# Kernel tuning notes

Hardware: AMD Instinct MI355X
Metric: run time of the kernel (lower is better)

Reference implementation:

```python
import jax, jax.numpy as jnp
import numpy as np

N, F, C, H, D = 32768, 128, 4, 8, 32
DM = H * D  # 256, d_model
E, B = 65536, 8192


def _pe():
    # sinusoidal positional encoding over the chain dimension, shape [C, DM]
    pos = jnp.arange(C, dtype=jnp.float32)[:, None]
    di = jnp.arange(0, DM, 2, dtype=jnp.float32)[None, :]
    div = 10000.0 ** (di / DM)
    pe = jnp.zeros((C, DM), jnp.float32)
    pe = pe.at[:, 0::2].set(jnp.sin(pos / div))
    pe = pe.at[:, 1::2].set(jnp.cos(pos / div))
    return pe


def _leaky(v):
    return jnp.where(v >= 0, v, 0.2 * v)


def setup_inputs() -> dict:
    key = jax.random.key(0)
    ks = jax.random.split(key, 6)
    x = jax.random.normal(ks[0], (N, F), jnp.float32)
    edge_index = jax.random.randint(ks[1], (2, E), 0, N)
    bridge_index = jax.random.randint(ks[2], (2, B), 0, N)
    W_in = jax.random.normal(ks[3], (DM, F), jnp.float32) * 0.05       # linear_input.weight
    double_attn = jax.random.normal(ks[4], (1, C * H, D), jnp.float32) * 0.1
    W_res = jax.random.normal(ks[5], (C * DM, F), jnp.float32) * 0.05  # residual_linear.weight
    bias = jnp.zeros((C * DM,), jnp.float32)
    prelu_w = jnp.float32(0.25)  # nn.PReLU default
    return {"x": x, "edge_index": edge_index, "bridge_index": bridge_index,
            "W_in": W_in, "double_attn": double_attn, "W_res": W_res,
            "bias": bias, "prelu_w": prelu_w}


def reference(x, edge_index, bridge_index, W_in, double_attn, W_res, bias, prelu_w):
    n = x.shape[0]
    # project + chain positional encoding -> [n, C, H, D]
    xl = x @ W_in.T                                   # [n, DM]
    xr = (xl[:, None, :] + _pe()[None]).reshape(n, C, H, D)

    src_bond, dst_bond = edge_index[0], edge_index[1]
    bond_attn = _leaky(xr[src_bond] + xr[dst_bond])   # [E, C, H, D]

    src_bridge, dst_bridge = bridge_index[0], bridge_index[1]
    ch = jnp.arange(C)
    prev_ch = jnp.clip(ch - 1, 0, None)
    next_ch = jnp.clip(ch + 1, None, C - 1)
    src2dst = _leaky(xr[dst_bridge] + xr[src_bridge][:, next_ch]).at[:, -1].set(0.0)
    dst2src = _leaky(xr[src_bridge] + xr[dst_bridge][:, prev_ch]).at[:, 0].set(0.0)

    full_src = jnp.concatenate([src_bond, src_bridge, dst_bridge])   # [Et]
    full_dst = jnp.concatenate([dst_bond, dst_bridge, src_bridge])   # [Et]
    x_src = jnp.concatenate([xr[src_bond], xr[src_bridge], xr[dst_bridge]], axis=0).reshape(-1, C * H, D)
    edge_attn = jnp.concatenate([bond_attn, src2dst, dst2src], axis=0).reshape(-1, C * H, D)

    scores = (double_attn * edge_attn).sum(-1)        # [Et, C*H]
    exp_s = jnp.exp(scores - scores.max())            # global-max stabilized, as in original
    denom = jax.ops.segment_sum(exp_s, full_dst, num_segments=n)     # [n, C*H]
    alpha = exp_s / (denom[full_dst] + 1e-16)

    # NOTE: faithful to original bug - x_src (per-edge, len Et) indexed by NODE ids
    proj = x_src[full_src] * alpha[..., None]         # [Et, C*H, D]
    out = jax.ops.segment_sum(proj, full_dst, num_segments=n)        # [n, C*H, D]

    out = out + (x @ W_res.T).reshape(n, C * H, D)    # residual
    out = out.reshape(n, C * H * D) + bias            # concat + bias
    out = jnp.where(out >= 0, out, prelu_w * out)     # PReLU
    return out
```

## Files before the change

### kernel.cpp

```cpp
#include <hip/hip_runtime.h>
#include <math.h>

#define N_NODES 32768
#define F_IN    128
#define C_CH    4
#define H_HEADS 8
#define D_DIM   32
#define DM      256
#define E_BOND  65536
#define B_BRIDGE 8192
#define ET      (E_BOND + 2*B_BRIDGE)
#define OUTC    1024
#define CAP     24
#define NCOLS   1280

#define WS_XL      0u
#define WS_XLB     33554432u
#define WS_PE      50331648u
#define WS_SCORES  50335744u
#define WS_BUCKET2 60821504u
#define WS_CNT     67112960u
#define WS_GMAX    67244032u
#define WS_RESID   67248128u
#define WS_XB      134356992u
#define WS_WC      142745600u

typedef __attribute__((ext_vector_type(8))) short bf16x8;
typedef __attribute__((ext_vector_type(4))) float f32x4;
typedef __attribute__((ext_vector_type(4))) _Float16 f16x4;

__device__ __forceinline__ unsigned enc_f32(float f) {
    unsigned u = __float_as_uint(f);
    return (u & 0x80000000u) ? ~u : (u | 0x80000000u);
}
__device__ __forceinline__ float dec_f32(unsigned u) {
    return (u & 0x80000000u) ? __uint_as_float(u & 0x7fffffffu) : __uint_as_float(~u);
}
__device__ __forceinline__ float leaky(float v) { return v >= 0.f ? v : 0.2f*v; }
__device__ __forceinline__ ushort f2bf(float f) {
    unsigned u = __float_as_uint(f);
    unsigned r = (u + 0x7fffu + ((u >> 16) & 1u)) >> 16;
    return (ushort)r;
}
__device__ __forceinline__ float bf2f(ushort u) {
    return __uint_as_float((unsigned)u << 16);
}

__device__ __forceinline__ void edge_decode(int e, const int* __restrict__ ei,
                                            const int* __restrict__ bi,
                                            int& nA, int& nB, int& tp) {
    if (e < E_BOND)               { nA = ei[e]; nB = ei[E_BOND + e]; tp = 0; }
    else if (e < E_BOND+B_BRIDGE) { int i = e - E_BOND;
                                    nA = bi[B_BRIDGE + i]; nB = bi[i]; tp = 1; }
    else                          { int i = e - E_BOND - B_BRIDGE;
                                    nA = bi[i]; nB = bi[B_BRIDGE + i]; tp = 2; }
}

__global__ void pe_init_kernel(float* __restrict__ pe, unsigned* __restrict__ gmax) {
    int tid = threadIdx.x;
    int c = tid >> 8, p = tid & 255;
    float expo = (float)(p & ~1) * (1.0f/256.0f);
    float div  = powf(10000.0f, expo);
    float arg  = (float)c / div;
    pe[tid] = (p & 1) ? cosf(arg) : sinf(arg);
    if (tid == 0) *gmax = 0u;
}

__global__ __launch_bounds__(256) void cvt_x_kernel(const float* __restrict__ x,
                                                    ushort* __restrict__ xb) {
    const long i = (long)blockIdx.x*256 + threadIdx.x;
    float4 v = ((const float4*)x)[i];
    ushort4 o; o.x = f2bf(v.x); o.y = f2bf(v.y); o.z = f2bf(v.z); o.w = f2bf(v.w);
    ((ushort4*)xb)[i] = o;
}
__global__ __launch_bounds__(256) void cvt_w_kernel(const float* __restrict__ W_in,
                                                    const float* __restrict__ W_res,
                                                    ushort* __restrict__ wc) {
    const int i = blockIdx.x*256 + threadIdx.x;
    float4 v = (i < 8192) ? ((const float4*)W_in)[i] : ((const float4*)W_res)[i - 8192];
    ushort4 o; o.x = f2bf(v.x); o.y = f2bf(v.y); o.z = f2bf(v.z); o.w = f2bf(v.w);
    ((ushort4*)wc)[i] = o;
}

#define LDSK 72
__global__ __launch_bounds__(256) void mfma_gemm(
        const ushort* __restrict__ xb, const ushort* __restrict__ wc,
        float* __restrict__ xl, ushort* __restrict__ xlb,
        _Float16* __restrict__ resid) {
    __shared__ ushort As[128*LDSK];
    __shared__ ushort Bs[128*LDSK];
    const int tid = threadIdx.x;
    const int m0 = blockIdx.x * 128;
    const int n0 = blockIdx.y * 128;
    const int lane = tid & 63, wv = tid >> 6;
    const int wm = wv & 1, wn = wv >> 1;
    const int quad = lane >> 4, l15 = lane & 15;
    const int mbase = wm*64, nbase = wn*64;
    f32x4 acc[4][4] = {};

    for (int kt = 0; kt < 2; ++kt) {
        if (kt) __syncthreads();
#pragma unroll
        for (int i = 0; i < 4; ++i) {
            int c = tid + i*256;
            int row = c >> 3, seg = c & 7;
            *(uint4*)&As[row*LDSK + seg*8] =
                *(const uint4*)(xb + (long)(m0 + row)*F_IN + kt*64 + seg*8);
        }
#pragma unroll
        for (int i = 0; i < 4; ++i) {
            int c = tid + i*256;
            int row = c >> 3, seg = c & 7;
            *(uint4*)&Bs[row*LDSK + seg*8] =
                *(const uint4*)(wc + (long)(n0 + row)*F_IN + kt*64 + seg*8);
        }
        __syncthreads();
#pragma unroll
        for (int ks = 0; ks < 2; ++ks) {
            const int ko = ks*32 + quad*8;
            bf16x8 af[4], bfr[4];
#pragma unroll
            for (int mi = 0; mi < 4; ++mi)
                af[mi] = *(const bf16x8*)&As[(mbase + mi*16 + l15)*LDSK + ko];
#pragma unroll
            for (int ni = 0; ni < 4; ++ni)
                bfr[ni] = *(const bf16x8*)&Bs[(nbase + ni*16 + l15)*LDSK + ko];
#pragma unroll
            for (int mi = 0; mi < 4; ++mi)
#pragma unroll
                for (int ni = 0; ni < 4; ++ni)
                    acc[mi][ni] = __builtin_amdgcn_mfma_f32_16x16x32_bf16(
                        af[mi], bfr[ni], acc[mi][ni], 0, 0, 0);
        }
    }

    if (n0 < DM) {
#pragma unroll
        for (int mi = 0; mi < 4; ++mi) {
            const int mrow = m0 + mbase + mi*16 + quad*4;
#pragma unroll
            for (int ni = 0; ni < 4; ++ni) {
                const int col = n0 + nbase + ni*16 + l15;
#pragma unroll
                for (int r = 0; r < 4; ++r) {
                    float v = acc[mi][ni][r];
                    xl [(long)(mrow + r)*DM + col] = v;
                    xlb[(long)(mrow + r)*DM + col] = f2bf(v);
                }
            }
        }
    } else {
        const int coloff = n0 - DM;
#pragma unroll
        for (int mi = 0; mi < 4; ++mi) {
            const int mrow = m0 + mbase + mi*16 + quad*4;
#pragma unroll
            for (int ni = 0; ni < 4; ++ni) {
                const int col = coloff + nbase + ni*16 + l15;
#pragma unroll
                for (int r = 0; r < 4; ++r)
                    resid[(long)(mrow + r)*OUTC + col] = (_Float16)acc[mi][ni][r];
            }
        }
    }
}

__global__ __launch_bounds__(256) void build_kernel(
        const int* __restrict__ ei, const int* __restrict__ bi,
        int* __restrict__ counts, int2* __restrict__ bucket2) {
    const int e = blockIdx.x*256 + threadIdx.x;
    if (e >= ET) return;
    int nA, nB, tp;
    edge_decode(e, ei, bi, nA, nB, tp);
    const int dst = (tp == 0) ? nB : nA;
    const int fs  = (tp == 0) ? nA : nB;
    const int g   = ei[fs];
    int slot = atomicAdd(&counts[dst], 1);
    if (slot < CAP) bucket2[dst*CAP + slot] = make_int2(e, g);
}

__global__ __launch_bounds__(256) void scores_kernel(
        const ushort* __restrict__ xlb, const float* __restrict__ pe,
        const int* __restrict__ ei, const int* __restrict__ bi,
        const float* __restrict__ datt, float* __restrict__ scores,
        unsigned* __restrict__ gmax) {
    const int tid = threadIdx.x;
    const int l = tid & 63, wv = tid >> 6;
    const int pos = l * 4;
    const int h = l >> 3, dq = l & 7;

    float4 pe4[4], w4[4];
#pragma unroll
    for (int c = 0; c < 4; ++c) {
        pe4[c] = *(const float4*)(pe + c*DM + pos);
        w4[c]  = *(const float4*)(datt + (c*H_HEADS + h)*D_DIM + dq*4);
    }

    float wmax = -1e30f;
    const int wavebase = (blockIdx.x*4 + wv) * 8;
#pragma unroll
    for (int gdx = 0; gdx < 2; ++gdx) {
        const int e0 = wavebase + gdx*4;
        int nA[4], nB[4], tp[4];
#pragma unroll
        for (int j = 0; j < 4; ++j)
            edge_decode(e0 + j, ei, bi, nA[j], nB[j], tp[j]);
        ushort4 ua[4], ub[4];
#pragma unroll
        for (int j = 0; j < 4; ++j) {
            ua[j] = *(const ushort4*)(xlb + (long)nA[j]*DM + pos);
            ub[j] = *(const ushort4*)(xlb + (long)nB[j]*DM + pos);
        }
#pragma unroll
        for (int j = 0; j < 4; ++j) {
            const int e = e0 + j, t = tp[j];
            float sx = bf2f(ua[j].x) + bf2f(ub[j].x);
            float sy = bf2f(ua[j].y) + bf2f(ub[j].y);
            float sz = bf2f(ua[j].z) + bf2f(ub[j].z);
            float sw = bf2f(ua[j].w) + bf2f(ub[j].w);

            float p[4];
#pragma unroll
            for (int c = 0; c < 4; ++c) {
                int cB = (t == 0) ? c : (t == 1 ? (c+1 < 3 ? c+1 : 3)
                                               : (c-1 > 0 ? c-1 : 0));
                bool z = (t == 1 && c == 3) || (t == 2 && c == 0);
                float4 pa = pe4[c];
                float4 pb = (cB == 0) ? pe4[0] : (cB == 1) ? pe4[1]
                           : (cB == 2) ? pe4[2] : pe4[3];
                float v0 = leaky(sx + pa.x + pb.x);
                float v1 = leaky(sy + pa.y + pb.y);
                float v2 = leaky(sz + pa.z + pb.z);
                float v3 = leaky(sw + pa.w + pb.w);
                float d = w4[c].x*v0 + w4[c].y*v1 + w4[c].z*v2 + w4[c].w*v3;
                p[c] = z ? 0.f : d;
                p[c] += __shfl_xor(p[c], 1);
                p[c] += __shfl_xor(p[c], 2);
                p[c] += __shfl_xor(p[c], 4);
            }
            float val = (dq == 0) ? p[0] : (dq == 1) ? p[1] : (dq == 2) ? p[2] : p[3];
            if (dq < 4) scores[(long)e*32 + dq*8 + h] = val;
            wmax = fmaxf(wmax, fmaxf(fmaxf(p[0], p[1]), fmaxf(p[2], p[3])));
        }
    }

    wmax = fmaxf(wmax, __shfl_xor(wmax, 8));
    wmax = fmaxf(wmax, __shfl_xor(wmax, 16));
    wmax = fmaxf(wmax, __shfl_xor(wmax, 32));
    __shared__ float sm[4];
    if (l == 0) sm[wv] = wmax;
    __syncthreads();
    if (tid == 0) {
        float mm = fmaxf(fmaxf(sm[0], sm[1]), fmaxf(sm[2], sm[3]));
        atomicMax(gmax, enc_f32(mm));
    }
}

__global__ __launch_bounds__(256) void alpha_kernel(
        const int* __restrict__ counts, const int2* __restrict__ bucket2,
        const unsigned* __restrict__ gmax, float* __restrict__ scores) {
    const int t = threadIdx.x;
    const int n = blockIdx.x*8 + (t >> 5);
    const int ch = t & 31;
    const float m = dec_f32(*gmax);
    const int cnt = min(counts[n], CAP);

    float ex[CAP];
    float den = 0.f;
#pragma unroll
    for (int i = 0; i < CAP; ++i) {
        if (i < cnt) {
            int e = bucket2[n*CAP + i].x;
            float v = __expf(scores[(long)e*32 + ch] - m);
            ex[i] = v; den += v;
        }
    }
    const float inv = 1.f / (den + 1e-16f);
#pragma unroll
    for (int i = 0; i < CAP; ++i) {
        if (i < cnt) {
            int e = bucket2[n*CAP + i].x;
            scores[(long)e*32 + ch] = ex[i] * inv;
        }
    }
}

__global__ __launch_bounds__(256) void gather_kernel(
        const float* __restrict__ xl, const float* __restrict__ pe,
        const float* __restrict__ alpha, const int* __restrict__ counts,
        const int2* __restrict__ bucket2, const _Float16* __restrict__ resid,
        const float* __restrict__ bias, const float* __restrict__ pw,
        float* __restrict__ out) {
    const int n = blockIdx.x;
    const int t = threadIdx.x;
    const int ch = t >> 3;
    const int d0 = (t & 7) * 4;
    const int h = ch & 7, c = ch >> 3;
    const int cnt = min(counts[n], CAP);
    const int col = ch*D_DIM + d0;
    const int nb = n*CAP;

    const f16x4 hv = *(const f16x4*)(resid + (long)n*OUTC + col);
    const float4 b = *(const float4*)(bias + col);
    const float w = *pw;
    const float4 pv = *(const float4*)(pe + c*DM + h*D_DIM + d0);

    float4 acc = make_float4(0.f, 0.f, 0.f, 0.f);
    float asum = 0.f;

    for (int i0 = 0; i0 < cnt; i0 += 4) {
#pragma unroll
        for (int j = 0; j < 4; ++j) {
            const int idx = i0 + j;
            const int safe = idx < cnt ? idx : i0;
            int2 eg = bucket2[nb + safe];
            float a = (idx < cnt) ? alpha[(long)eg.x*32 + ch] : 0.f;
            float4 xv = *(const float4*)(xl + (long)eg.y*DM + h*D_DIM + d0);
            acc.x += a*xv.x; acc.y += a*xv.y; acc.z += a*xv.z; acc.w += a*xv.w;
            asum += a;
        }
    }
    acc.x += asum*pv.x; acc.y += asum*pv.y; acc.z += asum*pv.z; acc.w += asum*pv.w;

    float r0 = acc.x + (float)hv.x + b.x;
    float r1 = acc.y + (float)hv.y + b.y;
    float r2 = acc.z + (float)hv.z + b.z;
    float r3 = acc.w + (float)hv.w + b.w;
    r0 = r0 >= 0.f ? r0 : w*r0;
    r1 = r1 >= 0.f ? r1 : w*r1;
    r2 = r2 >= 0.f ? r2 : w*r2;
    r3 = r3 >= 0.f ? r3 : w*r3;
    *(float4*)(out + (long)n*OUTC + col) = make_float4(r0, r1, r2, r3);
}

extern "C" void kernel_launch(void* const* d_in, const int* in_sizes, int n_in,
                              void* d_out, int out_size, void* d_ws, size_t ws_size,
                              hipStream_t stream) {
    const float* x     = (const float*)d_in[0];
    const int*   ei    = (const int*)d_in[1];
    const int*   bi    = (const int*)d_in[2];
    const float* W_in  = (const float*)d_in[3];
    const float* datt  = (const float*)d_in[4];
    const float* W_res = (const float*)d_in[5];
    const float* bias  = (const float*)d_in[6];
    const float* pw    = (const float*)d_in[7];
    float* out = (float*)d_out;
    char*  ws  = (char*)d_ws;

    float*     xl      = (float*)(ws + WS_XL);
    ushort*    xlb     = (ushort*)(ws + WS_XLB);
    float*     pe      = (float*)(ws + WS_PE);
    float*     scores  = (float*)(ws + WS_SCORES);
    int2*      bucket2 = (int2*)(ws + WS_BUCKET2);
    int*       counts  = (int*)(ws + WS_CNT);
    unsigned*  gmax    = (unsigned*)(ws + WS_GMAX);
    _Float16*  resid   = (_Float16*)(ws + WS_RESID);
    ushort*    xb      = (ushort*)(ws + WS_XB);
    ushort*    wc      = (ushort*)(ws + WS_WC);

    hipMemsetAsync(counts, 0, (size_t)N_NODES*4, stream);
    pe_init_kernel<<<1, 1024, 0, stream>>>(pe, gmax);
    cvt_x_kernel<<<(N_NODES*F_IN/4)/256, 256, 0, stream>>>(x, xb);
    cvt_w_kernel<<<(NCOLS*F_IN/4 + 255)/256, 256, 0, stream>>>(W_in, W_res, wc);
    build_kernel<<<(ET+255)/256, 256, 0, stream>>>(ei, bi, counts, bucket2);
    {
        dim3 grid(N_NODES/128, NCOLS/128);
        mfma_gemm<<<grid, 256, 0, stream>>>(xb, wc, xl, xlb, resid);
    }
    scores_kernel<<<2560, 256, 0, stream>>>(xlb, pe, ei, bi, datt, scores, gmax);
    alpha_kernel<<<N_NODES/8, 256, 0, stream>>>(counts, bucket2, gmax, scores);
    gather_kernel<<<N_NODES, 256, 0, stream>>>(xl, pe, scores, counts, bucket2,
                                               resid, bias, pw, out);
}
```

Measured before the change: 345.6 us.

## Fuse score, softmax and gather into one per-node kernel with local max

Replaces the separate scores, alpha and gather kernels with a single node-centric kernel that computes edge scores for each destination's bucket, does the softmax in shared memory, and aggregates. The bucket now stores source/dest node ids and edge type, so the global per-edge scores buffer and the global atomic max are removed. Softmax stabilization uses a per-node max instead of the global max, which is mathematically equivalent. Normalization is applied once after accumulation. In exchange, the score phase per block has low parallelism for small degrees.

```diff
diff --git a/kernel.cpp b/kernel.cpp
--- a/kernel.cpp
+++ b/kernel.cpp
@@ -17,25 +17,16 @@
 #define WS_XL      0u
 #define WS_XLB     33554432u
 #define WS_PE      50331648u
-#define WS_SCORES  50335744u
-#define WS_BUCKET2 60821504u
-#define WS_CNT     67112960u
-#define WS_GMAX    67244032u
-#define WS_RESID   67248128u
-#define WS_XB      134356992u
-#define WS_WC      142745600u
+#define WS_BUCKET  50335744u
+#define WS_CNT     62918656u
+#define WS_RESID   63049728u
+#define WS_XB      130158592u
+#define WS_WC      138547200u
 
 typedef __attribute__((ext_vector_type(8))) short bf16x8;
 typedef __attribute__((ext_vector_type(4))) float f32x4;
 typedef __attribute__((ext_vector_type(4))) _Float16 f16x4;
 
-__device__ __forceinline__ unsigned enc_f32(float f) {
-    unsigned u = __float_as_uint(f);
-    return (u & 0x80000000u) ? ~u : (u | 0x80000000u);
-}
-__device__ __forceinline__ float dec_f32(unsigned u) {
-    return (u & 0x80000000u) ? __uint_as_float(u & 0x7fffffffu) : __uint_as_float(~u);
-}
 __device__ __forceinline__ float leaky(float v) { return v >= 0.f ? v : 0.2f*v; }
 __device__ __forceinline__ ushort f2bf(float f) {
     unsigned u = __float_as_uint(f);
@@ -56,14 +47,13 @@
                                     nA = bi[i]; nB = bi[B_BRIDGE + i]; tp = 2; }
 }
 
-__global__ void pe_init_kernel(float* __restrict__ pe, unsigned* __restrict__ gmax) {
+__global__ void pe_init_kernel(float* __restrict__ pe) {
     int tid = threadIdx.x;
     int c = tid >> 8, p = tid & 255;
     float expo = (float)(p & ~1) * (1.0f/256.0f);
     float div  = powf(10000.0f, expo);
     float arg  = (float)c / div;
     pe[tid] = (p & 1) ? cosf(arg) : sinf(arg);
-    if (tid == 0) *gmax = 0u;
 }
 
 __global__ __launch_bounds__(256) void cvt_x_kernel(const float* __restrict__ x,
@@ -167,7 +157,7 @@
 
 __global__ __launch_bounds__(256) void build_kernel(
         const int* __restrict__ ei, const int* __restrict__ bi,
-        int* __restrict__ counts, int2* __restrict__ bucket2) {
+        int* __restrict__ counts, int4* __restrict__ bucket4) {
     const int e = blockIdx.x*256 + threadIdx.x;
     if (e >= ET) return;
     int nA, nB, tp;
@@ -176,55 +166,50 @@
     const int fs  = (tp == 0) ? nA : nB;
     const int g   = ei[fs];
     int slot = atomicAdd(&counts[dst], 1);
-    if (slot < CAP) bucket2[dst*CAP + slot] = make_int2(e, g);
-}
-
-__global__ __launch_bounds__(256) void scores_kernel(
-        const ushort* __restrict__ xlb, const float* __restrict__ pe,
-        const int* __restrict__ ei, const int* __restrict__ bi,
-        const float* __restrict__ datt, float* __restrict__ scores,
-        unsigned* __restrict__ gmax) {
-    const int tid = threadIdx.x;
-    const int l = tid & 63, wv = tid >> 6;
-    const int pos = l * 4;
-    const int h = l >> 3, dq = l & 7;
-
-    float4 pe4[4], w4[4];
-#pragma unroll
-    for (int c = 0; c < 4; ++c) {
-        pe4[c] = *(const float4*)(pe + c*DM + pos);
-        w4[c]  = *(const float4*)(datt + (c*H_HEADS + h)*D_DIM + dq*4);
-    }
-
-    float wmax = -1e30f;
-    const int wavebase = (blockIdx.x*4 + wv) * 8;
-#pragma unroll
-    for (int gdx = 0; gdx < 2; ++gdx) {
-        const int e0 = wavebase + gdx*4;
-        int nA[4], nB[4], tp[4];
-#pragma unroll
-        for (int j = 0; j < 4; ++j)
-            edge_decode(e0 + j, ei, bi, nA[j], nB[j], tp[j]);
-        ushort4 ua[4], ub[4];
-#pragma unroll
-        for (int j = 0; j < 4; ++j) {
-            ua[j] = *(const ushort4*)(xlb + (long)nA[j]*DM + pos);
-            ub[j] = *(const ushort4*)(xlb + (long)nB[j]*DM + pos);
-        }
-#pragma unroll
-        for (int j = 0; j < 4; ++j) {
-            const int e = e0 + j, t = tp[j];
-            float sx = bf2f(ua[j].x) + bf2f(ub[j].x);
-            float sy = bf2f(ua[j].y) + bf2f(ub[j].y);
-            float sz = bf2f(ua[j].z) + bf2f(ub[j].z);
-            float sw = bf2f(ua[j].w) + bf2f(ub[j].w);
+    if (slot < CAP) bucket4[(long)dst*CAP + slot] = make_int4(nA, nB, g, tp);
+}
+
+__global__ __launch_bounds__(256) void node_kernel(
+        const float* __restrict__ xl, const ushort* __restrict__ xlb,
+        const float* __restrict__ pe, const float* __restrict__ datt,
+        const int* __restrict__ counts, const int4* __restrict__ bucket4,
+        const _Float16* __restrict__ resid, const float* __restrict__ bias,
+        const float* __restrict__ pw, float* __restrict__ out) {
+    __shared__ float s_sc[CAP][32];
+    __shared__ int   s_g[CAP];
+    __shared__ float s_inv[32];
+
+    const int n = blockIdx.x;
+    const int t = threadIdx.x;
+    const int l = t & 63, wv = t >> 6;
+    const int cnt = min(counts[n], CAP);
+
+    {
+        const int pos = l * 4;
+        const int h8 = l >> 3, dq = l & 7;
+        float4 pe4[4], w4[4];
+#pragma unroll
+        for (int c = 0; c < 4; ++c) {
+            pe4[c] = *(const float4*)(pe + c*DM + pos);
+            w4[c]  = *(const float4*)(datt + (c*H_HEADS + h8)*D_DIM + dq*4);
+        }
+        for (int i = wv; i < cnt; i += 4) {
+            const int4 ed = bucket4[(long)n*CAP + i];
+            if (l == 0) s_g[i] = ed.z;
+            const int tp = ed.w;
+            ushort4 ua = *(const ushort4*)(xlb + (long)ed.x*DM + pos);
+            ushort4 ub = *(const ushort4*)(xlb + (long)ed.y*DM + pos);
+            float sx = bf2f(ua.x) + bf2f(ub.x);
+            float sy = bf2f(ua.y) + bf2f(ub.y);
+            float sz = bf2f(ua.z) + bf2f(ub.z);
+            float sw = bf2f(ua.w) + bf2f(ub.w);
 
             float p[4];
 #pragma unroll
             for (int c = 0; c < 4; ++c) {
-                int cB = (t == 0) ? c : (t == 1 ? (c+1 < 3 ? c+1 : 3)
-                                               : (c-1 > 0 ? c-1 : 0));
-                bool z = (t == 1 && c == 3) || (t == 2 && c == 0);
+                int cB = (tp == 0) ? c : (tp == 1 ? (c+1 < 3 ? c+1 : 3)
+                                                  : (c-1 > 0 ? c-1 : 0));
+                bool z = (tp == 1 && c == 3) || (tp == 2 && c == 0);
                 float4 pa = pe4[c];
                 float4 pb = (cB == 0) ? pe4[0] : (cB == 1) ? pe4[1]
                            : (cB == 2) ? pe4[2] : pe4[3];
@@ -238,94 +223,53 @@
                 p[c] += __shfl_xor(p[c], 2);
                 p[c] += __shfl_xor(p[c], 4);
             }
-            float val = (dq == 0) ? p[0] : (dq == 1) ? p[1] : (dq == 2) ? p[2] : p[3];
-            if (dq < 4) scores[(long)e*32 + dq*8 + h] = val;
-            wmax = fmaxf(wmax, fmaxf(fmaxf(p[0], p[1]), fmaxf(p[2], p[3])));
-        }
-    }
-
-    wmax = fmaxf(wmax, __shfl_xor(wmax, 8));
-    wmax = fmaxf(wmax, __shfl_xor(wmax, 16));
-    wmax = fmaxf(wmax, __shfl_xor(wmax, 32));
-    __shared__ float sm[4];
-    if (l == 0) sm[wv] = wmax;
+            if (dq < 4) {
+                float val = (dq == 0) ? p[0] : (dq == 1) ? p[1]
+                           : (dq == 2) ? p[2] : p[3];
+                s_sc[i][dq*8 + h8] = val;
+            }
+        }
+    }
     __syncthreads();
-    if (tid == 0) {
-        float mm = fmaxf(fmaxf(sm[0], sm[1]), fmaxf(sm[2], sm[3]));
-        atomicMax(gmax, enc_f32(mm));
-    }
-}
-
-__global__ __launch_bounds__(256) void alpha_kernel(
-        const int* __restrict__ counts, const int2* __restrict__ bucket2,
-        const unsigned* __restrict__ gmax, float* __restrict__ scores) {
-    const int t = threadIdx.x;
-    const int n = blockIdx.x*8 + (t >> 5);
-    const int ch = t & 31;
-    const float m = dec_f32(*gmax);
-    const int cnt = min(counts[n], CAP);
-
-    float ex[CAP];
-    float den = 0.f;
-#pragma unroll
-    for (int i = 0; i < CAP; ++i) {
-        if (i < cnt) {
-            int e = bucket2[n*CAP + i].x;
-            float v = __expf(scores[(long)e*32 + ch] - m);
-            ex[i] = v; den += v;
-        }
-    }
-    const float inv = 1.f / (den + 1e-16f);
-#pragma unroll
-    for (int i = 0; i < CAP; ++i) {
-        if (i < cnt) {
-            int e = bucket2[n*CAP + i].x;
-            scores[(long)e*32 + ch] = ex[i] * inv;
-        }
-    }
-}
-
-__global__ __launch_bounds__(256) void gather_kernel(
-        const float* __restrict__ xl, const float* __restrict__ pe,
-        const float* __restrict__ alpha, const int* __restrict__ counts,
-        const int2* __restrict__ bucket2, const _Float16* __restrict__ resid,
-        const float* __restrict__ bias, const float* __restrict__ pw,
-        float* __restrict__ out) {
-    const int n = blockIdx.x;
-    const int t = threadIdx.x;
+
+    if (t < 32) {
+        float m = -1e30f;
+        for (int i = 0; i < cnt; ++i) m = fmaxf(m, s_sc[i][t]);
+        float den = 0.f;
+        for (int i = 0; i < cnt; ++i) {
+            float v = __expf(s_sc[i][t] - m);
+            s_sc[i][t] = v;
+            den += v;
+        }
+        s_inv[t] = 1.f / (den + 1e-16f);
+    }
+    __syncthreads();
+
     const int ch = t >> 3;
     const int d0 = (t & 7) * 4;
-    const int h = ch & 7, c = ch >> 3;
-    const int cnt = min(counts[n], CAP);
+    const int hh = ch & 7, cc = ch >> 3;
+    const int dmoff = hh*D_DIM + d0;
     const int col = ch*D_DIM + d0;
-    const int nb = n*CAP;
 
     const f16x4 hv = *(const f16x4*)(resid + (long)n*OUTC + col);
     const float4 b = *(const float4*)(bias + col);
     const float w = *pw;
-    const float4 pv = *(const float4*)(pe + c*DM + h*D_DIM + d0);
+    const float4 pv = *(const float4*)(pe + cc*DM + dmoff);
 
     float4 acc = make_float4(0.f, 0.f, 0.f, 0.f);
     float asum = 0.f;
-
-    for (int i0 = 0; i0 < cnt; i0 += 4) {
-#pragma unroll
-        for (int j = 0; j < 4; ++j) {
-            const int idx = i0 + j;
-            const int safe = idx < cnt ? idx : i0;
-            int2 eg = bucket2[nb + safe];
-            float a = (idx < cnt) ? alpha[(long)eg.x*32 + ch] : 0.f;
-            float4 xv = *(const float4*)(xl + (long)eg.y*DM + h*D_DIM + d0);
-            acc.x += a*xv.x; acc.y += a*xv.y; acc.z += a*xv.z; acc.w += a*xv.w;
-            asum += a;
-        }
-    }
-    acc.x += asum*pv.x; acc.y += asum*pv.y; acc.z += asum*pv.z; acc.w += asum*pv.w;
-
-    float r0 = acc.x + (float)hv.x + b.x;
-    float r1 = acc.y + (float)hv.y + b.y;
-    float r2 = acc.z + (float)hv.z + b.z;
-    float r3 = acc.w + (float)hv.w + b.w;
+    for (int i = 0; i < cnt; ++i) {
+        float a = s_sc[i][ch];
+        int g = s_g[i];
+        float4 xv = *(const float4*)(xl + (long)g*DM + dmoff);
+        acc.x += a*xv.x; acc.y += a*xv.y; acc.z += a*xv.z; acc.w += a*xv.w;
+        asum += a;
+    }
+    const float inv = s_inv[ch];
+    float r0 = (acc.x + asum*pv.x)*inv + (float)hv.x + b.x;
+    float r1 = (acc.y + asum*pv.y)*inv + (float)hv.y + b.y;
+    float r2 = (acc.z + asum*pv.z)*inv + (float)hv.z + b.z;
+    float r3 = (acc.w + asum*pv.w)*inv + (float)hv.w + b.w;
     r0 = r0 >= 0.f ? r0 : w*r0;
     r1 = r1 >= 0.f ? r1 : w*r1;
     r2 = r2 >= 0.f ? r2 : w*r2;
@@ -350,25 +294,21 @@
     float*     xl      = (float*)(ws + WS_XL);
     ushort*    xlb     = (ushort*)(ws + WS_XLB);
     float*     pe      = (float*)(ws + WS_PE);
-    float*     scores  = (float*)(ws + WS_SCORES);
-    int2*      bucket2 = (int2*)(ws + WS_BUCKET2);
+    int4*      bucket4 = (int4*)(ws + WS_BUCKET);
     int*       counts  = (int*)(ws + WS_CNT);
-    unsigned*  gmax    = (unsigned*)(ws + WS_GMAX);
     _Float16*  resid   = (_Float16*)(ws + WS_RESID);
     ushort*    xb      = (ushort*)(ws + WS_XB);
     ushort*    wc      = (ushort*)(ws + WS_WC);
 
     hipMemsetAsync(counts, 0, (size_t)N_NODES*4, stream);
-    pe_init_kernel<<<1, 1024, 0, stream>>>(pe, gmax);
+    pe_init_kernel<<<1, 1024, 0, stream>>>(pe);
     cvt_x_kernel<<<(N_NODES*F_IN/4)/256, 256, 0, stream>>>(x, xb);
     cvt_w_kernel<<<(NCOLS*F_IN/4 + 255)/256, 256, 0, stream>>>(W_in, W_res, wc);
-    build_kernel<<<(ET+255)/256, 256, 0, stream>>>(ei, bi, counts, bucket2);
+    build_kernel<<<(ET+255)/256, 256, 0, stream>>>(ei, bi, counts, bucket4);
     {
         dim3 grid(N_NODES/128, NCOLS/128);
         mfma_gemm<<<grid, 256, 0, stream>>>(xb, wc, xl, xlb, resid);
     }
-    scores_kernel<<<2560, 256, 0, stream>>>(xlb, pe, ei, bi, datt, scores, gmax);
-    alpha_kernel<<<N_NODES/8, 256, 0, stream>>>(counts, bucket2, gmax, scores);
-    gather_kernel<<<N_NODES, 256, 0, stream>>>(xl, pe, scores, counts, bucket2,
-                                               resid, bias, pw, out);
-}
+    node_kernel<<<N_NODES, 256, 0, stream>>>(xl, xlb, pe, datt, counts, bucket4,
+                                             resid, bias, pw, out);
+}
```

After: 415.7 us. 20.3% more time.

## Fuse softmax normalization into gather and drop bf16 copy of projected features

Applied to the files above, without the earlier changes.

Removes the separate alpha kernel: the gather kernel now computes exp(score - global max) on the fly, accumulates the unnormalized weighted sum and the exponent sum, and divides once at the end. It also drops the bf16 copy of xl written by the GEMM, so the scores kernel reads fp32 xl directly. This saves one kernel launch, a full read-modify-write pass over scores, and the extra bf16 store traffic. In exchange, the scores kernel gathers twice as many bytes per edge.

```diff
diff --git a/kernel.cpp b/kernel.cpp
--- a/kernel.cpp
+++ b/kernel.cpp
@@ -15,15 +15,14 @@
 #define NCOLS   1280
 
 #define WS_XL      0u
-#define WS_XLB     33554432u
-#define WS_PE      50331648u
-#define WS_SCORES  50335744u
-#define WS_BUCKET2 60821504u
-#define WS_CNT     67112960u
-#define WS_GMAX    67244032u
-#define WS_RESID   67248128u
-#define WS_XB      134356992u
-#define WS_WC      142745600u
+#define WS_PE      33554432u
+#define WS_SCORES  33558528u
+#define WS_BUCKET2 44044288u
+#define WS_CNT     50335744u
+#define WS_GMAX    50466816u
+#define WS_RESID   50470912u
+#define WS_XB      117579776u
+#define WS_WC      125968384u
 
 typedef __attribute__((ext_vector_type(8))) short bf16x8;
 typedef __attribute__((ext_vector_type(4))) float f32x4;
@@ -41,9 +40,6 @@
     unsigned u = __float_as_uint(f);
     unsigned r = (u + 0x7fffu + ((u >> 16) & 1u)) >> 16;
     return (ushort)r;
-}
-__device__ __forceinline__ float bf2f(ushort u) {
-    return __uint_as_float((unsigned)u << 16);
 }
 
 __device__ __forceinline__ void edge_decode(int e, const int* __restrict__ ei,
@@ -85,8 +81,7 @@
 #define LDSK 72
 __global__ __launch_bounds__(256) void mfma_gemm(
         const ushort* __restrict__ xb, const ushort* __restrict__ wc,
-        float* __restrict__ xl, ushort* __restrict__ xlb,
-        _Float16* __restrict__ resid) {
+        float* __restrict__ xl, _Float16* __restrict__ resid) {
     __shared__ ushort As[128*LDSK];
     __shared__ ushort Bs[128*LDSK];
     const int tid = threadIdx.x;
@@ -142,11 +137,8 @@
             for (int ni = 0; ni < 4; ++ni) {
                 const int col = n0 + nbase + ni*16 + l15;
 #pragma unroll
-                for (int r = 0; r < 4; ++r) {
-                    float v = acc[mi][ni][r];
-                    xl [(long)(mrow + r)*DM + col] = v;
-                    xlb[(long)(mrow + r)*DM + col] = f2bf(v);
-                }
+                for (int r = 0; r < 4; ++r)
+                    xl[(long)(mrow + r)*DM + col] = acc[mi][ni][r];
             }
         }
     } else {
@@ -180,7 +172,7 @@
 }
 
 __global__ __launch_bounds__(256) void scores_kernel(
-        const ushort* __restrict__ xlb, const float* __restrict__ pe,
+        const float* __restrict__ xl, const float* __restrict__ pe,
         const int* __restrict__ ei, const int* __restrict__ bi,
         const float* __restrict__ datt, float* __restrict__ scores,
         unsigned* __restrict__ gmax) {
@@ -205,19 +197,19 @@
 #pragma unroll
         for (int j = 0; j < 4; ++j)
             edge_decode(e0 + j, ei, bi, nA[j], nB[j], tp[j]);
-        ushort4 ua[4], ub[4];
+        float4 ua[4], ub[4];
 #pragma unroll
         for (int j = 0; j < 4; ++j) {
-            ua[j] = *(const ushort4*)(xlb + (long)nA[j]*DM + pos);
-            ub[j] = *(const ushort4*)(xlb + (long)nB[j]*DM + pos);
+            ua[j] = *(const float4*)(xl + (long)nA[j]*DM + pos);
+            ub[j] = *(const float4*)(xl + (long)nB[j]*DM + pos);
         }
 #pragma unroll
         for (int j = 0; j < 4; ++j) {
             const int e = e0 + j, t = tp[j];
-            float sx = bf2f(ua[j].x) + bf2f(ub[j].x);
-            float sy = bf2f(ua[j].y) + bf2f(ub[j].y);
-            float sz = bf2f(ua[j].z) + bf2f(ub[j].z);
-            float sw = bf2f(ua[j].w) + bf2f(ub[j].w);
+            float sx = ua[j].x + ub[j].x;
+            float sy = ua[j].y + ub[j].y;
+            float sz = ua[j].z + ub[j].z;
+            float sw = ua[j].w + ub[j].w;
 
             float p[4];
 #pragma unroll
@@ -256,41 +248,12 @@
     }
 }
 
-__global__ __launch_bounds__(256) void alpha_kernel(
-        const int* __restrict__ counts, const int2* __restrict__ bucket2,
-        const unsigned* __restrict__ gmax, float* __restrict__ scores) {
-    const int t = threadIdx.x;
-    const int n = blockIdx.x*8 + (t >> 5);
-    const int ch = t & 31;
-    const float m = dec_f32(*gmax);
-    const int cnt = min(counts[n], CAP);
-
-    float ex[CAP];
-    float den = 0.f;
-#pragma unroll
-    for (int i = 0; i < CAP; ++i) {
-        if (i < cnt) {
-            int e = bucket2[n*CAP + i].x;
-            float v = __expf(scores[(long)e*32 + ch] - m);
-            ex[i] = v; den += v;
-        }
-    }
-    const float inv = 1.f / (den + 1e-16f);
-#pragma unroll
-    for (int i = 0; i < CAP; ++i) {
-        if (i < cnt) {
-            int e = bucket2[n*CAP + i].x;
-            scores[(long)e*32 + ch] = ex[i] * inv;
-        }
-    }
-}
-
 __global__ __launch_bounds__(256) void gather_kernel(
         const float* __restrict__ xl, const float* __restrict__ pe,
-        const float* __restrict__ alpha, const int* __restrict__ counts,
+        const float* __restrict__ scores, const int* __restrict__ counts,
         const int2* __restrict__ bucket2, const _Float16* __restrict__ resid,
-        const float* __restrict__ bias, const float* __restrict__ pw,
-        float* __restrict__ out) {
+        const unsigned* __restrict__ gmax, const float* __restrict__ bias,
+        const float* __restrict__ pw, float* __restrict__ out) {
     const int n = blockIdx.x;
     const int t = threadIdx.x;
     const int ch = t >> 3;
@@ -299,6 +262,7 @@
     const int cnt = min(counts[n], CAP);
     const int col = ch*D_DIM + d0;
     const int nb = n*CAP;
+    const float m = dec_f32(*gmax);
 
     const f16x4 hv = *(const f16x4*)(resid + (long)n*OUTC + col);
     const float4 b = *(const float4*)(bias + col);
@@ -306,26 +270,39 @@
     const float4 pv = *(const float4*)(pe + c*DM + h*D_DIM + d0);
 
     float4 acc = make_float4(0.f, 0.f, 0.f, 0.f);
-    float asum = 0.f;
+    float esum = 0.f;
 
     for (int i0 = 0; i0 < cnt; i0 += 4) {
+        int2 eg[4]; bool vld[4];
 #pragma unroll
         for (int j = 0; j < 4; ++j) {
             const int idx = i0 + j;
             const int safe = idx < cnt ? idx : i0;
-            int2 eg = bucket2[nb + safe];
-            float a = (idx < cnt) ? alpha[(long)eg.x*32 + ch] : 0.f;
-            float4 xv = *(const float4*)(xl + (long)eg.y*DM + h*D_DIM + d0);
-            acc.x += a*xv.x; acc.y += a*xv.y; acc.z += a*xv.z; acc.w += a*xv.w;
-            asum += a;
-        }
-    }
-    acc.x += asum*pv.x; acc.y += asum*pv.y; acc.z += asum*pv.z; acc.w += asum*pv.w;
-
-    float r0 = acc.x + (float)hv.x + b.x;
-    float r1 = acc.y + (float)hv.y + b.y;
-    float r2 = acc.z + (float)hv.z + b.z;
-    float r3 = acc.w + (float)hv.w + b.w;
+            eg[j] = bucket2[nb + safe];
+            vld[j] = idx < cnt;
+        }
+        float sc[4];
+#pragma unroll
+        for (int j = 0; j < 4; ++j)
+            sc[j] = scores[(long)eg[j].x*32 + ch];
+        float4 xv[4];
+#pragma unroll
+        for (int j = 0; j < 4; ++j)
+            xv[j] = *(const float4*)(xl + (long)eg[j].y*DM + h*D_DIM + d0);
+#pragma unroll
+        for (int j = 0; j < 4; ++j) {
+            float ex = vld[j] ? __expf(sc[j] - m) : 0.f;
+            acc.x += ex*xv[j].x; acc.y += ex*xv[j].y;
+            acc.z += ex*xv[j].z; acc.w += ex*xv[j].w;
+            esum += ex;
+        }
+    }
+    const float inv = 1.f / (esum + 1e-16f);
+
+    float r0 = (acc.x + esum*pv.x)*inv + (float)hv.x + b.x;
+    float r1 = (acc.y + esum*pv.y)*inv + (float)hv.y + b.y;
+    float r2 = (acc.z + esum*pv.z)*inv + (float)hv.z + b.z;
+    float r3 = (acc.w + esum*pv.w)*inv + (float)hv.w + b.w;
     r0 = r0 >= 0.f ? r0 : w*r0;
     r1 = r1 >= 0.f ? r1 : w*r1;
     r2 = r2 >= 0.f ? r2 : w*r2;
@@ -348,7 +325,6 @@
     char*  ws  = (char*)d_ws;
 
     float*     xl      = (float*)(ws + WS_XL);
-    ushort*    xlb     = (ushort*)(ws + WS_XLB);
     float*     pe      = (float*)(ws + WS_PE);
     float*     scores  = (float*)(ws + WS_SCORES);
     int2*      bucket2 = (int2*)(ws + WS_BUCKET2);
@@ -365,10 +341,9 @@
     build_kernel<<<(ET+255)/256, 256, 0, stream>>>(ei, bi, counts, bucket2);
     {
         dim3 grid(N_NODES/128, NCOLS/128);
-        mfma_gemm<<<grid, 256, 0, stream>>>(xb, wc, xl, xlb, resid);
-    }
-    scores_kernel<<<2560, 256, 0, stream>>>(xlb, pe, ei, bi, datt, scores, gmax);
-    alpha_kernel<<<N_NODES/8, 256, 0, stream>>>(counts, bucket2, gmax, scores);
+        mfma_gemm<<<grid, 256, 0, stream>>>(xb, wc, xl, resid);
+    }
+    scores_kernel<<<2560, 256, 0, stream>>>(xl, pe, ei, bi, datt, scores, gmax);
     gather_kernel<<<N_NODES, 256, 0, stream>>>(xl, pe, scores, counts, bucket2,
-                                               resid, bias, pw, out);
-}
+                                               resid, gmax, bias, pw, out);
+}
```

Result: faster. 321.7 us (-6.9%).
